# Kernel optimization log

Measured on AMD Instinct MI355X. Metric: run time of the kernel, lower is better.

## Reference

```python
import jax, jax.numpy as jnp
import numpy as np

C = 1.0                      # curvature
PHI = 3.1415926 * 0.3        # Cosine phase (bias=False path)
ALPHA = 0.2                  # LeakyReLU negative slope
A_PARA = 0.5                 # a_para_GATLayer
EPS = 4e-3                   # float32 ball-projection epsilon (standard HGCN)
MIN_NORM = 1e-15
NEG_INF = -9e15              # matches -9000000000000000.0 in source


def project(x, c):
    # clamp points to lie inside the Poincare ball of curvature c
    norm = jnp.maximum(jnp.linalg.norm(x, axis=-1, keepdims=True), MIN_NORM)
    maxnorm = (1.0 - EPS) / jnp.sqrt(c)
    return jnp.where(norm > maxnorm, x / norm * maxnorm, x)


def artanh(x):
    return jnp.arctanh(jnp.clip(x, -1.0 + 1e-7, 1.0 - 1e-7))


def logmap0(p, c):
    # log map at the origin of the Poincare ball
    sqrt_c = c ** 0.5
    p_norm = jnp.maximum(jnp.linalg.norm(p, axis=-1, keepdims=True), MIN_NORM)
    return artanh(sqrt_c * p_norm) / (sqrt_c * p_norm) * p


def setup_inputs() -> dict:
    key = jax.random.key(0)
    k1, k2, k3, k4 = jax.random.split(key, 4)
    N, FIN, FOUT = 8192, 512, 128
    h = jax.random.normal(k1, (N, FIN), dtype=jnp.float32)
    adj = jax.random.randint(k2, (N, N), 0, 2, dtype=jnp.int32)
    # xavier_uniform with gain=1.414
    lim_w = 1.414 * np.sqrt(6.0 / (FIN + FOUT))
    W = jax.random.uniform(k3, (FIN, FOUT), jnp.float32, -lim_w, lim_w)
    lim_a = 1.414 * np.sqrt(6.0 / (2 * FOUT + 1))
    a = jax.random.uniform(k4, (2 * FOUT, 1), jnp.float32, -lim_a, lim_a)
    return {"h": h, "adj": adj, "W": W, "a": a}


def reference(h, adj, W, a):
    fout = W.shape[1]
    Wh = h @ W                                   # [N, F_out]
    Wh1 = Wh @ a[:fout]                          # [N, 1] source score
    Wh2 = Wh @ a[fout:]                          # [N, 1] target score
    e = jax.nn.leaky_relu(Wh1 + Wh2.T, ALPHA)    # [N, N]
    e = jnp.where(adj > 0, e, NEG_INF)
    attention = jax.nn.softmax(e, axis=1)        # dropout p=0 (eval): identity
    h_prime = attention @ Wh                     # [N, F_out]
    h_prime = logmap0(project(h_prime, C), C)
    # concat=True branch: ELU + a_para * A*cos(x + phi), A=1 (data_dim=-1)
    return jax.nn.elu(h_prime) + A_PARA * jnp.cos(h_prime + PHI)
```

## Files before the change

kernel.cpp:

```cpp
#include <hip/hip_runtime.h>
#include <hip/hip_bf16.h>
#include <math.h>

typedef short short8 __attribute__((ext_vector_type(8)));
typedef float f32x4 __attribute__((ext_vector_type(4)));

static constexpr int N = 8192;
static constexpr int FIN = 512;
static constexpr int FOUT = 128;
static constexpr int NJC = 8;
static constexpr float PHI = 3.1415926f * 0.3f;
static constexpr float A_PARA = 0.5f;
static constexpr float EPS_BALL = 4e-3f;
static constexpr float L2E = 1.4426950408889634f;

__device__ __forceinline__ unsigned short f2b(float f) {
    union { float f; unsigned u; } v; v.f = f;
    unsigned r = v.u + 0x7fffu + ((v.u >> 16) & 1u);
    return (unsigned short)(r >> 16);
}

__device__ __forceinline__ short f2bn(float f) {
    __hip_bfloat16 h = __float2bfloat16(f);
    return *reinterpret_cast<short*>(&h);
}

__device__ __forceinline__ unsigned f2key(float x) {
    unsigned b = __float_as_uint(x);
    return (b & 0x80000000u) ? ~b : (b | 0x80000000u);
}
__device__ __forceinline__ float key2f(unsigned k) {
    unsigned b = (k & 0x80000000u) ? (k ^ 0x80000000u) : ~k;
    return __uint_as_float(b);
}

__device__ __forceinline__ short8 cvt8(float4 x0, float4 x1) {
    short8 r;
    r[0] = (short)f2b(x0.x); r[1] = (short)f2b(x0.y);
    r[2] = (short)f2b(x0.z); r[3] = (short)f2b(x0.w);
    r[4] = (short)f2b(x1.x); r[5] = (short)f2b(x1.y);
    r[6] = (short)f2b(x1.z); r[7] = (short)f2b(x1.w);
    return r;
}

__device__ __forceinline__ void cw(float* w, const int4 a, const float4 tv,
                                   float sA, float mA) {
    float z;
    z = sA + tv.x; w[0] = a.x > 0 ? __builtin_amdgcn_exp2f(fmaxf(z, 0.2f * z) - mA) : 0.f;
    z = sA + tv.y; w[1] = a.y > 0 ? __builtin_amdgcn_exp2f(fmaxf(z, 0.2f * z) - mA) : 0.f;
    z = sA + tv.z; w[2] = a.z > 0 ? __builtin_amdgcn_exp2f(fmaxf(z, 0.2f * z) - mA) : 0.f;
    z = sA + tv.w; w[3] = a.w > 0 ? __builtin_amdgcn_exp2f(fmaxf(z, 0.2f * z) - mA) : 0.f;
}

__global__ __launch_bounds__(256) void k0_wt(const float* __restrict__ W,
                                             unsigned short* __restrict__ Wt,
                                             unsigned* __restrict__ Tkey,
                                             float* __restrict__ denb) {
    __shared__ float sh[32][33];
    const int t = threadIdx.x;
    const int k0 = (blockIdx.x >> 2) * 32, c0 = (blockIdx.x & 3) * 32;
    {
        int r = t >> 3, c4 = (t & 7) * 4;
        float4 v = *(const float4*)(W + (size_t)(k0 + r) * FOUT + c0 + c4);
        sh[r][c4] = v.x; sh[r][c4 + 1] = v.y; sh[r][c4 + 2] = v.z; sh[r][c4 + 3] = v.w;
    }
    __syncthreads();
    int cc = t >> 3, k4 = (t & 7) * 4;
    ushort4 o;
    o.x = f2b(sh[k4][cc]); o.y = f2b(sh[k4 + 1][cc]);
    o.z = f2b(sh[k4 + 2][cc]); o.w = f2b(sh[k4 + 3][cc]);
    *(ushort4*)(Wt + (size_t)(c0 + cc) * FIN + k0 + k4) = o;
    if (blockIdx.x == 0) {
        if (t == 0) Tkey[0] = 0u;
        for (int i = t; i < N; i += 256) denb[i] = 0.f;
    }
}

__global__ __launch_bounds__(256) void k1_gemm(
    const float* __restrict__ h, const unsigned short* __restrict__ Wt,
    const float* __restrict__ a, unsigned short* __restrict__ whbt,
    float* __restrict__ s_out, float* __restrict__ t_out,
    unsigned* __restrict__ Tkey)
{
    __shared__ unsigned short wlds[128][520];
    __shared__ unsigned short hsb[2][32][72];
    __shared__ float sred[32][2], tred[32][2];
    const int t = threadIdx.x, lane = t & 63, wave = t >> 6;
    const int i0 = blockIdx.x * 32;
    const int wr = wave & 1, wc = wave >> 1;
    const int arow = lane & 15, g = lane >> 4;
    const int sr = t >> 3, sc = (t & 7) * 8;
    const float* hp = h + (size_t)(i0 + sr) * FIN + sc;

    for (int idx = t; idx < (FOUT * FIN) / 8; idx += 256) {
        const int row = idx >> 6, col = (idx & 63) * 8;
        *(short8*)&wlds[row][col] = *(const short8*)(Wt + (size_t)row * FIN + col);
    }
    float4 x0 = *(const float4*)hp, x1 = *(const float4*)(hp + 4);
    *(short8*)&hsb[0][sr][sc] = cvt8(x0, x1);
    __syncthreads();

    f32x4 acc[4];
    const f32x4 zz = {0.f, 0.f, 0.f, 0.f};
    #pragma unroll
    for (int cf = 0; cf < 4; ++cf) acc[cf] = zz;

    #pragma unroll 1
    for (int kt = 0; kt < 8; ++kt) {
        const int cur = kt & 1;
        float4 y0, y1;
        if (kt < 7) {
            y0 = *(const float4*)(hp + (kt + 1) * 64);
            y1 = *(const float4*)(hp + (kt + 1) * 64 + 4);
        }
        #pragma unroll
        for (int js = 0; js < 64; js += 32) {
            short8 af = *(const short8*)&hsb[cur][wr * 16 + arow][js + g * 8];
            #pragma unroll
            for (int cf = 0; cf < 4; ++cf) {
                short8 bf = *(const short8*)&wlds[wc * 64 + cf * 16 + arow][kt * 64 + js + g * 8];
                acc[cf] = __builtin_amdgcn_mfma_f32_16x16x32_bf16(af, bf, acc[cf], 0, 0, 0);
            }
        }
        if (kt < 7) {
            *(short8*)&hsb[cur ^ 1][sr][sc] = cvt8(y0, y1);
            __syncthreads();
        }
    }

    float a1v[4], a2v[4];
    #pragma unroll
    for (int cf = 0; cf < 4; ++cf) {
        int col = wc * 64 + cf * 16 + arow;
        a1v[cf] = a[col]; a2v[cf] = a[FOUT + col];
    }
    #pragma unroll
    for (int cf = 0; cf < 4; ++cf) {
        int col = wc * 64 + cf * 16 + arow;
        ushort4 o;
        o.x = f2b(acc[cf][0]); o.y = f2b(acc[cf][1]);
        o.z = f2b(acc[cf][2]); o.w = f2b(acc[cf][3]);
        *(ushort4*)(whbt + (size_t)col * N + i0 + wr * 16 + g * 4) = o;
    }
    #pragma unroll
    for (int q = 0; q < 4; ++q) {
        float sp = acc[0][q]*a1v[0] + acc[1][q]*a1v[1] + acc[2][q]*a1v[2] + acc[3][q]*a1v[3];
        float tp = acc[0][q]*a2v[0] + acc[1][q]*a2v[1] + acc[2][q]*a2v[2] + acc[3][q]*a2v[3];
        #pragma unroll
        for (int m = 1; m < 16; m <<= 1) {
            sp += __shfl_xor(sp, m, 16);
            tp += __shfl_xor(tp, m, 16);
        }
        if (arow == 0) {
            sred[wr * 16 + g * 4 + q][wc] = sp;
            tred[wr * 16 + g * 4 + q][wc] = tp;
        }
    }
    __syncthreads();
    if (t < 32) {
        float sp = (sred[t][0] + sred[t][1]) * L2E;
        float tp = (tred[t][0] + tred[t][1]) * L2E;
        s_out[i0 + t] = sp;
        t_out[i0 + t] = tp;
        float m = tp;
        #pragma unroll
        for (int d = 1; d < 32; d <<= 1) m = fmaxf(m, __shfl_xor(m, d, 32));
        if (t == 0) atomicMax(Tkey, f2key(m));
    }
}

__global__ __launch_bounds__(512, 4) void k3_attn(
    const int* __restrict__ adj, const unsigned short* __restrict__ whbt,
    const float* __restrict__ s_in, const float* __restrict__ t_in,
    const unsigned* __restrict__ Tkey,
    unsigned short* __restrict__ num_bf, float* __restrict__ num_f32,
    float* __restrict__ den_out, int slice_mode)
{
    __shared__ unsigned short bt[2][128][72];
    __shared__ float tl[1024];
    const int t = threadIdx.x, lane = t & 63, wave = t >> 6;
    const int jc = blockIdx.x & (NJC - 1), it = blockIdx.x / NJC;
    const int i0 = it * 128, jbase = jc * (N / NJC);

    tl[t] = t_in[jbase + t];
    tl[t + 512] = t_in[jbase + t + 512];

    const int arow = lane & 15, g = lane >> 4;
    const int grow = i0 + wave * 16 + arow;
    const float sA = s_in[grow];
    const float Tv = key2f(Tkey[0]);
    const float zT = sA + Tv;
    const float mA = fmaxf(zT, 0.2f * zT);
    const int* adjrow = adj + (size_t)grow * N;
    const int srow = t >> 2, scol = (t & 3) * 16;
    const unsigned short* sbase = whbt + (size_t)srow * N + jbase + scol;

    f32x4 acc[8];
    const f32x4 zz = {0.f, 0.f, 0.f, 0.f};
    #pragma unroll
    for (int c = 0; c < 8; ++c) acc[c] = zz;
    float den = 0.f;

    short8 s00 = *(const short8*)sbase;
    short8 s01 = *(const short8*)(sbase + 8);
    short8 nc0 = *(const short8*)(sbase + 64);
    short8 nc1 = *(const short8*)(sbase + 72);
    int4 av0 = *(const int4*)(adjrow + jbase + g * 8);
    int4 av1 = *(const int4*)(adjrow + jbase + g * 8 + 4);
    int4 av2 = *(const int4*)(adjrow + jbase + 32 + g * 8);
    int4 av3 = *(const int4*)(adjrow + jbase + 32 + g * 8 + 4);
    *(short8*)&bt[0][srow][scol]     = s00;
    *(short8*)&bt[0][srow][scol + 8] = s01;
    __syncthreads();

    #pragma unroll 1
    for (int jt = 0; jt < 16; ++jt) {
        const int cur = jt & 1, jl = jt * 64;
        const int jt2 = (jt + 2 < 16) ? jt + 2 : 15;
        short8 nn0, nn1;
        {
            const unsigned short* p = sbase + jt2 * 64;
            nn0 = *(const short8*)p;
            nn1 = *(const short8*)(p + 8);
        }
        const int jt1 = (jt + 1 < 16) ? jt + 1 : 15;
        int4 an0, an1, an2, an3;
        {
            const int* ap = adjrow + jbase + jt1 * 64;
            an0 = *(const int4*)(ap + g * 8);
            an1 = *(const int4*)(ap + g * 8 + 4);
            an2 = *(const int4*)(ap + 32 + g * 8);
            an3 = *(const int4*)(ap + 32 + g * 8 + 4);
        }
        float4 ta = *(const float4*)&tl[jl + g * 8];
        float4 tb = *(const float4*)&tl[jl + g * 8 + 4];
        float4 tc = *(const float4*)&tl[jl + 32 + g * 8];
        float4 td = *(const float4*)&tl[jl + 32 + g * 8 + 4];
        float w[16];
        cw(&w[0],  av0, ta, sA, mA);
        cw(&w[4],  av1, tb, sA, mA);
        cw(&w[8],  av2, tc, sA, mA);
        cw(&w[12], av3, td, sA, mA);
        #pragma unroll
        for (int e = 0; e < 16; ++e) den += w[e];
        short8 af0, af1;
        #pragma unroll
        for (int e = 0; e < 8; ++e) {
            af0[e] = f2bn(w[e]);
            af1[e] = f2bn(w[8 + e]);
        }
        #pragma unroll
        for (int c = 0; c < 8; ++c) {
            short8 bf = *(const short8*)&bt[cur][c * 16 + arow][g * 8];
            acc[c] = __builtin_amdgcn_mfma_f32_16x16x32_bf16(af0, bf, acc[c], 0, 0, 0);
        }
        #pragma unroll
        for (int c = 0; c < 8; ++c) {
            short8 bf = *(const short8*)&bt[cur][c * 16 + arow][32 + g * 8];
            acc[c] = __builtin_amdgcn_mfma_f32_16x16x32_bf16(af1, bf, acc[c], 0, 0, 0);
        }
        if (jt < 15) {
            *(short8*)&bt[cur ^ 1][srow][scol]     = nc0;
            *(short8*)&bt[cur ^ 1][srow][scol + 8] = nc1;
            nc0 = nn0; nc1 = nn1;
            av0 = an0; av1 = an1; av2 = an2; av3 = an3;
            __syncthreads();
        }
    }

    den += __shfl_xor(den, 16, 64);
    den += __shfl_xor(den, 32, 64);
    if (g == 0) atomicAdd(&den_out[grow], den);

    const int orow0 = i0 + wave * 16;
    if (slice_mode) {
        unsigned short* dst = num_bf + (size_t)jc * ((size_t)N * FOUT);
        #pragma unroll
        for (int c = 0; c < 8; ++c)
            #pragma unroll
            for (int q = 0; q < 4; ++q)
                dst[(size_t)(orow0 + g * 4 + q) * FOUT + c * 16 + arow] = f2b(acc[c][q]);
    } else {
        #pragma unroll
        for (int c = 0; c < 8; ++c)
            #pragma unroll
            for (int q = 0; q < 4; ++q)
                atomicAdd(&num_f32[(size_t)(orow0 + g * 4 + q) * FOUT + c * 16 + arow], acc[c][q]);
    }
}

__global__ __launch_bounds__(256) void k4_epi(
    const unsigned short* __restrict__ numb, const float* __restrict__ numf,
    const float* __restrict__ den, float* __restrict__ out, int bfmode)
{
    const int row = blockIdx.x * 16 + (threadIdx.x >> 4);
    const int col0 = (threadIdx.x & 15) * 8;
    const float inv = 1.0f / den[row];
    float v[8] = {};
    if (bfmode) {
        #pragma unroll 1
        for (int s5 = 0; s5 < NJC; ++s5) {
            short8 b = *(const short8*)(numb + (size_t)s5 * N * FOUT + (size_t)row * FOUT + col0);
            #pragma unroll
            for (int c = 0; c < 8; ++c)
                v[c] += __uint_as_float(((unsigned)(unsigned short)b[c]) << 16);
        }
    } else {
        #pragma unroll
        for (int c = 0; c < 8; ++c) v[c] = numf[(size_t)row * FOUT + col0 + c];
    }
    float ss = 0.f;
    #pragma unroll
    for (int c = 0; c < 8; ++c) { v[c] *= inv; ss += v[c] * v[c]; }
    #pragma unroll
    for (int m = 1; m < 16; m <<= 1) ss += __shfl_xor(ss, m, 16);
    float nrm = sqrtf(ss);
    const float maxn = 1.0f - EPS_BALL;
    float scale1 = nrm > maxn ? maxn / nrm : 1.0f;
    float pn = fminf(nrm, maxn);
    float fac;
    if (pn < 1e-6f) fac = scale1;
    else fac = scale1 * (0.5f * __logf((1.f + pn) / (1.f - pn))) / pn;
    float o[8];
    #pragma unroll
    for (int c = 0; c < 8; ++c) {
        float hv = v[c] * fac;
        float eluv = hv > 0.f ? hv : __expf(hv) - 1.f;
        o[c] = eluv + A_PARA * __cosf(hv + PHI);
    }
    float* op = out + (size_t)row * FOUT + col0;
    *(float4*)op = make_float4(o[0], o[1], o[2], o[3]);
    *(float4*)(op + 4) = make_float4(o[4], o[5], o[6], o[7]);
}

extern "C" void kernel_launch(void* const* d_in, const int* in_sizes, int n_in,
                              void* d_out, int out_size, void* d_ws, size_t ws_size,
                              hipStream_t stream) {
    const float* h   = (const float*)d_in[0];
    const int*   adj = (const int*)d_in[1];
    const float* W   = (const float*)d_in[2];
    const float* a   = (const float*)d_in[3];
    float* out = (float*)d_out;

    char* ws = (char*)d_ws;
    unsigned short* whbt = (unsigned short*)ws;
    size_t off = (size_t)N * FOUT * 2;
    unsigned short* Wt = (unsigned short*)(ws + off); off += (size_t)FOUT * FIN * 2;
    float* s  = (float*)(ws + off); off += (size_t)N * 4;
    float* tt = (float*)(ws + off); off += (size_t)N * 4;
    unsigned* Tkey = (unsigned*)(ws + off); off += 256;
    float* denb = (float*)(ws + off); off += (size_t)N * 4;
    const size_t slice_bytes = (size_t)N * FOUT * 2;
    const bool fast = ws_size >= off + (size_t)NJC * slice_bytes;
    unsigned short* numb = fast ? (unsigned short*)(ws + off) : nullptr;

    if (!fast) hipMemsetAsync(out, 0, (size_t)N * FOUT * 4, stream);

    k0_wt<<<64, 256, 0, stream>>>(W, Wt, Tkey, denb);
    k1_gemm<<<N / 32, 256, 0, stream>>>(h, Wt, a, whbt, s, tt, Tkey);
    k3_attn<<<(N / 128) * NJC, 512, 0, stream>>>(adj, whbt, s, tt, Tkey, numb, out, denb, fast ? 1 : 0);
    k4_epi<<<N / 16, 256, 0, stream>>>(numb, out, denb, out, fast ? 1 : 0);
}
```

Before: 93.90 us.

## Switch attention kernel to 32x32x16 MFMA with 4x2 wave tiling

```diff
diff --git a/kernel.cpp b/kernel.cpp
--- a/kernel.cpp
+++ b/kernel.cpp
@@ -4,6 +4,7 @@
 
 typedef short short8 __attribute__((ext_vector_type(8)));
 typedef float f32x4 __attribute__((ext_vector_type(4)));
+typedef float f32x16 __attribute__((ext_vector_type(16)));
 
 static constexpr int N = 8192;
 static constexpr int FIN = 512;
@@ -176,7 +177,7 @@
     unsigned short* __restrict__ num_bf, float* __restrict__ num_f32,
     float* __restrict__ den_out, int slice_mode)
 {
-    __shared__ unsigned short bt[2][128][72];
+    __shared__ unsigned short bt[2][128][40];
     __shared__ float tl[1024];
     const int t = threadIdx.x, lane = t & 63, wave = t >> 6;
     const int jc = blockIdx.x & (NJC - 1), it = blockIdx.x / NJC;
@@ -185,62 +186,54 @@
     tl[t] = t_in[jbase + t];
     tl[t + 512] = t_in[jbase + t + 512];
 
-    const int arow = lane & 15, g = lane >> 4;
-    const int grow = i0 + wave * 16 + arow;
+    const int l31 = lane & 31, hi = lane >> 5, hi8 = hi * 8;
+    const int wrow = wave & 3, wcol = wave >> 2;
+    const int cb = wcol * 64;
+    const int grow = i0 + wrow * 32 + l31;
     const float sA = s_in[grow];
     const float Tv = key2f(Tkey[0]);
     const float zT = sA + Tv;
     const float mA = fmaxf(zT, 0.2f * zT);
     const int* adjrow = adj + (size_t)grow * N;
-    const int srow = t >> 2, scol = (t & 3) * 16;
-    const unsigned short* sbase = whbt + (size_t)srow * N + jbase + scol;
-
-    f32x4 acc[8];
-    const f32x4 zz = {0.f, 0.f, 0.f, 0.f};
-    #pragma unroll
-    for (int c = 0; c < 8; ++c) acc[c] = zz;
+    const int srow = t >> 2, jc8 = (t & 3) * 8;
+    const unsigned short* sbase = whbt + (size_t)srow * N + jbase + jc8;
+
+    f32x16 acc0 = {0.f,0.f,0.f,0.f,0.f,0.f,0.f,0.f,0.f,0.f,0.f,0.f,0.f,0.f,0.f,0.f};
+    f32x16 acc1 = acc0;
     float den = 0.f;
 
     short8 s00 = *(const short8*)sbase;
-    short8 s01 = *(const short8*)(sbase + 8);
-    short8 nc0 = *(const short8*)(sbase + 64);
-    short8 nc1 = *(const short8*)(sbase + 72);
-    int4 av0 = *(const int4*)(adjrow + jbase + g * 8);
-    int4 av1 = *(const int4*)(adjrow + jbase + g * 8 + 4);
-    int4 av2 = *(const int4*)(adjrow + jbase + 32 + g * 8);
-    int4 av3 = *(const int4*)(adjrow + jbase + 32 + g * 8 + 4);
-    *(short8*)&bt[0][srow][scol]     = s00;
-    *(short8*)&bt[0][srow][scol + 8] = s01;
+    short8 nc0 = *(const short8*)(sbase + 32);
+    int4 av0 = *(const int4*)(adjrow + jbase + hi8);
+    int4 av1 = *(const int4*)(adjrow + jbase + hi8 + 4);
+    int4 av2 = *(const int4*)(adjrow + jbase + 16 + hi8);
+    int4 av3 = *(const int4*)(adjrow + jbase + 16 + hi8 + 4);
+    *(short8*)&bt[0][srow][jc8] = s00;
     __syncthreads();
 
     #pragma unroll 1
-    for (int jt = 0; jt < 16; ++jt) {
-        const int cur = jt & 1, jl = jt * 64;
-        const int jt2 = (jt + 2 < 16) ? jt + 2 : 15;
-        short8 nn0, nn1;
-        {
-            const unsigned short* p = sbase + jt2 * 64;
-            nn0 = *(const short8*)p;
-            nn1 = *(const short8*)(p + 8);
-        }
-        const int jt1 = (jt + 1 < 16) ? jt + 1 : 15;
+    for (int jt = 0; jt < 32; ++jt) {
+        const int cur = jt & 1, jl = jt * 32;
+        const int jt2 = (jt + 2 < 32) ? jt + 2 : 31;
+        short8 nn0 = *(const short8*)(sbase + jt2 * 32);
+        const int jt1 = (jt + 1 < 32) ? jt + 1 : 31;
         int4 an0, an1, an2, an3;
         {
-            const int* ap = adjrow + jbase + jt1 * 64;
-            an0 = *(const int4*)(ap + g * 8);
-            an1 = *(const int4*)(ap + g * 8 + 4);
-            an2 = *(const int4*)(ap + 32 + g * 8);
-            an3 = *(const int4*)(ap + 32 + g * 8 + 4);
-        }
-        float4 ta = *(const float4*)&tl[jl + g * 8];
-        float4 tb = *(const float4*)&tl[jl + g * 8 + 4];
-        float4 tc = *(const float4*)&tl[jl + 32 + g * 8];
-        float4 td = *(const float4*)&tl[jl + 32 + g * 8 + 4];
+            const int* ap = adjrow + jbase + jt1 * 32;
+            an0 = *(const int4*)(ap + hi8);
+            an1 = *(const int4*)(ap + hi8 + 4);
+            an2 = *(const int4*)(ap + 16 + hi8);
+            an3 = *(const int4*)(ap + 16 + hi8 + 4);
+        }
+        float4 ta0 = *(const float4*)&tl[jl + hi8];
+        float4 ta1 = *(const float4*)&tl[jl + hi8 + 4];
+        float4 tb0 = *(const float4*)&tl[jl + 16 + hi8];
+        float4 tb1 = *(const float4*)&tl[jl + 16 + hi8 + 4];
         float w[16];
-        cw(&w[0],  av0, ta, sA, mA);
-        cw(&w[4],  av1, tb, sA, mA);
-        cw(&w[8],  av2, tc, sA, mA);
-        cw(&w[12], av3, td, sA, mA);
+        cw(&w[0],  av0, ta0, sA, mA);
+        cw(&w[4],  av1, ta1, sA, mA);
+        cw(&w[8],  av2, tb0, sA, mA);
+        cw(&w[12], av3, tb1, sA, mA);
         #pragma unroll
         for (int e = 0; e < 16; ++e) den += w[e];
         short8 af0, af1;
@@ -249,43 +242,43 @@
             af0[e] = f2bn(w[e]);
             af1[e] = f2bn(w[8 + e]);
         }
-        #pragma unroll
-        for (int c = 0; c < 8; ++c) {
-            short8 bf = *(const short8*)&bt[cur][c * 16 + arow][g * 8];
-            acc[c] = __builtin_amdgcn_mfma_f32_16x16x32_bf16(af0, bf, acc[c], 0, 0, 0);
-        }
-        #pragma unroll
-        for (int c = 0; c < 8; ++c) {
-            short8 bf = *(const short8*)&bt[cur][c * 16 + arow][32 + g * 8];
-            acc[c] = __builtin_amdgcn_mfma_f32_16x16x32_bf16(af1, bf, acc[c], 0, 0, 0);
-        }
-        if (jt < 15) {
-            *(short8*)&bt[cur ^ 1][srow][scol]     = nc0;
-            *(short8*)&bt[cur ^ 1][srow][scol + 8] = nc1;
-            nc0 = nn0; nc1 = nn1;
+        {
+            short8 bf00 = *(const short8*)&bt[cur][cb + l31][hi8];
+            short8 bf01 = *(const short8*)&bt[cur][cb + l31][16 + hi8];
+            short8 bf10 = *(const short8*)&bt[cur][cb + 32 + l31][hi8];
+            short8 bf11 = *(const short8*)&bt[cur][cb + 32 + l31][16 + hi8];
+            acc0 = __builtin_amdgcn_mfma_f32_32x32x16_bf16(af0, bf00, acc0, 0, 0, 0);
+            acc0 = __builtin_amdgcn_mfma_f32_32x32x16_bf16(af1, bf01, acc0, 0, 0, 0);
+            acc1 = __builtin_amdgcn_mfma_f32_32x32x16_bf16(af0, bf10, acc1, 0, 0, 0);
+            acc1 = __builtin_amdgcn_mfma_f32_32x32x16_bf16(af1, bf11, acc1, 0, 0, 0);
+        }
+        if (jt < 31) {
+            *(short8*)&bt[cur ^ 1][srow][jc8] = nc0;
+            nc0 = nn0;
             av0 = an0; av1 = an1; av2 = an2; av3 = an3;
             __syncthreads();
         }
     }
 
-    den += __shfl_xor(den, 16, 64);
     den += __shfl_xor(den, 32, 64);
-    if (g == 0) atomicAdd(&den_out[grow], den);
-
-    const int orow0 = i0 + wave * 16;
+    if (hi == 0 && wcol == 0) atomicAdd(&den_out[grow], den);
+
+    const int orow0 = i0 + wrow * 32;
     if (slice_mode) {
         unsigned short* dst = num_bf + (size_t)jc * ((size_t)N * FOUT);
         #pragma unroll
-        for (int c = 0; c < 8; ++c)
-            #pragma unroll
-            for (int q = 0; q < 4; ++q)
-                dst[(size_t)(orow0 + g * 4 + q) * FOUT + c * 16 + arow] = f2b(acc[c][q]);
+        for (int r = 0; r < 16; ++r) {
+            const int rowl = (r & 3) + 8 * (r >> 2) + 4 * hi;
+            dst[(size_t)(orow0 + rowl) * FOUT + cb + l31]      = f2b(acc0[r]);
+            dst[(size_t)(orow0 + rowl) * FOUT + cb + 32 + l31] = f2b(acc1[r]);
+        }
     } else {
         #pragma unroll
-        for (int c = 0; c < 8; ++c)
-            #pragma unroll
-            for (int q = 0; q < 4; ++q)
-                atomicAdd(&num_f32[(size_t)(orow0 + g * 4 + q) * FOUT + c * 16 + arow], acc[c][q]);
+        for (int r = 0; r < 16; ++r) {
+            const int rowl = (r & 3) + 8 * (r >> 2) + 4 * hi;
+            atomicAdd(&num_f32[(size_t)(orow0 + rowl) * FOUT + cb + l31], acc0[r]);
+            atomicAdd(&num_f32[(size_t)(orow0 + rowl) * FOUT + cb + 32 + l31], acc1[r]);
+        }
     }
 }
 
```

Measured after the change: 118.5 us. +26.2%, slower.
